# Optimization experiments

Measured on AMD Instinct MI355X. Metric: run time of the kernel, lower is better.

Reference implementation:

```python
import jax, jax.numpy as jnp
import numpy as np

DIM = 1024
STATE = 16
K = 4
INNER = 2048
BATCH = 4
SEQ = 2048
EPS = 1e-6


def silu(x):
    return x * jax.nn.sigmoid(x)


def setup_inputs() -> dict:
    key = jax.random.key(0)
    ks = jax.random.split(key, 8)
    g = lambda k, s, sc: jax.random.normal(k, s, dtype=jnp.float32) * sc
    return {
        "x": jax.random.normal(ks[0], (BATCH, SEQ, DIM), dtype=jnp.float32),
        "w_norm": jnp.ones((DIM,), jnp.float32),
        "W_in": g(ks[1], (2 * INNER, DIM), 0.02),
        "conv_w": g(ks[2], (INNER, K), 0.2),  # depthwise conv kernel
        "conv_b": jnp.zeros((INNER,), jnp.float32),
        "W_dt": g(ks[3], (INNER, INNER), 0.02),
        "b_dt": jnp.zeros((INNER,), jnp.float32),
        "W_B": g(ks[4], (STATE, INNER), 0.02),
        "W_C": g(ks[5], (STATE, INNER), 0.02),
        "A_log": jnp.log(jnp.broadcast_to(jnp.arange(1, STATE + 1, dtype=jnp.float32), (INNER, STATE))),
        "D": jnp.ones((INNER,), jnp.float32),
        "W_out": g(ks[6], (DIM, INNER), 0.02),
    }


def reference(x, w_norm, W_in, conv_w, conv_b, W_dt, b_dt, W_B, W_C, A_log, D, W_out):
    b, L, d = x.shape
    # RMSNorm
    x_norm = x * jax.lax.rsqrt(jnp.mean(x * x, axis=-1, keepdims=True) + EPS) * w_norm
    # input projection and split
    x_and_res = x_norm @ W_in.T  # (b, L, 2*inner)
    x_inner, res = jnp.split(x_and_res, 2, axis=-1)
    # causal depthwise conv1d (pad left K-1, kernel per channel)
    xp = jnp.pad(x_inner, ((0, 0), (K - 1, 0), (0, 0)))
    x_conv = sum(xp[:, j:j + L, :] * conv_w[:, j] for j in range(K)) + conv_b
    x_conv = silu(x_conv)
    # SSM parameters
    dt = jax.nn.softplus(x_conv @ W_dt.T + b_dt)  # (b, L, inner)
    Bm = x_conv @ W_B.T  # (b, L, state)
    Cm = x_conv @ W_C.T  # (b, L, state)
    A = -jnp.exp(A_log)  # (inner, state)

    def step(h, inp):
        dt_t, B_t, C_t, xc_t = inp  # (b,inner),(b,state),(b,state),(b,inner)
        dA = jnp.exp(A * dt_t[..., None])  # (b, inner, state)
        h = dA * h + (dt_t[..., None] * B_t[:, None, :]) * xc_t[..., None]
        y_t = jnp.einsum('bis,bs->bi', h, C_t) + D * xc_t
        return h, y_t

    h0 = jnp.zeros((b, INNER, STATE), x.dtype)
    xs = (dt.transpose(1, 0, 2), Bm.transpose(1, 0, 2), Cm.transpose(1, 0, 2), x_conv.transpose(1, 0, 2))
    _, y = jax.lax.scan(step, h0, xs)  # y: (L, b, inner)
    y = y.transpose(1, 0, 2)
    y = y * silu(res)
    return y @ W_out.T
```

## Files before the change

### kernel.cpp

```cpp
#include <hip/hip_runtime.h>


typedef __bf16 bf16;
typedef __attribute__((ext_vector_type(8))) __bf16 bf16x8;
typedef __attribute__((ext_vector_type(4))) float f32x4;

#define DIM   1024
#define STATE 16
#define INNER 2048
#define BATCH 4
#define SEQ   2048
#define ROWS  (BATCH * SEQ)
#define N1    (2 * INNER)
#define NBC   2176
#define CHUNK 128
#define NC    (SEQ / CHUNK)
#define PF2   4

#define GLOAD_LDS16(g, l)                                                  \
  __builtin_amdgcn_global_load_lds(                                        \
      (const __attribute__((address_space(1))) unsigned int*)(g),          \
      (__attribute__((address_space(3))) unsigned int*)(l), 16, 0, 0)

__global__ void ws_report_kernel(float* out, float wssz, float need) {
  if (threadIdx.x == 0) { out[0] = wssz; out[1] = need; }
}

__global__ __launch_bounds__(256) void rmsnorm_kernel(
    const float* __restrict__ x, const float* __restrict__ w,
    bf16* __restrict__ out) {
  const int row = blockIdx.x;
  const int t = threadIdx.x;
  const float4 v = ((const float4*)(x + (long)row * DIM))[t];
  float ss = v.x * v.x + v.y * v.y + v.z * v.z + v.w * v.w;
#pragma unroll
  for (int off = 32; off > 0; off >>= 1) ss += __shfl_xor(ss, off, 64);
  __shared__ float red[4];
  if ((t & 63) == 0) red[t >> 6] = ss;
  __syncthreads();
  const float tot = red[0] + red[1] + red[2] + red[3];
  const float scale = rsqrtf(tot * (1.0f / DIM) + 1e-6f);
  const float4 wv = ((const float4*)w)[t];
  bf16* o = out + (long)row * DIM + t * 4;
  o[0] = (bf16)(v.x * scale * wv.x);
  o[1] = (bf16)(v.y * scale * wv.y);
  o[2] = (bf16)(v.z * scale * wv.z);
  o[3] = (bf16)(v.w * scale * wv.w);
}

__global__ __launch_bounds__(256) void cvt_bf16_kernel(
    const float* __restrict__ src, bf16* __restrict__ dst, int n) {
  const int i = blockIdx.x * 256 + threadIdx.x;
  if (i < n) dst[i] = (bf16)src[i];
}

__global__ __launch_bounds__(256) void build_wbc_kernel(
    const float* __restrict__ WB, const float* __restrict__ WC,
    bf16* __restrict__ dst) {
  const int i = blockIdx.x * 256 + threadIdx.x;
  const int r = i >> 11;
  const int k = i & (INNER - 1);
  float v = 0.0f;
  if (r < 16) v = WB[r * INNER + k];
  else if (r < 32) v = WC[(r - 16) * INNER + k];
  dst[i] = (bf16)v;
}

__global__ __launch_bounds__(256) void build_a2_kernel(
    const float* __restrict__ A_log, float* __restrict__ A2) {
  const int i = blockIdx.x * 256 + threadIdx.x;
  A2[i] = -__expf(A_log[i]) * 1.4426950408889634f;
}

template <int EPI, int K, int NX>
__global__ __launch_bounds__(512, 2) void gemm256_kernel(
    const bf16* __restrict__ A, const bf16* __restrict__ B,
    float* __restrict__ Cf, bf16* __restrict__ Cb, bf16* __restrict__ Cb2,
    const float* __restrict__ bias) {
  __shared__ __align__(16) char lds[4][32768];
  const int tid = threadIdx.x;
  const int lane = tid & 63;
  const int wave = tid >> 6;
  const int wm = wave >> 2;
  const int wn = wave & 3;

  const int per = gridDim.x >> 3;
  const int lin = (blockIdx.x & 7) * per + (blockIdx.x >> 3);
  const int row_t = lin / NX;
  const int col_t = lin - row_t * NX;
  const long row0 = (long)row_t * 256;
  const long col0 = (long)col_t * 256;

  const int srow = tid >> 2;
  const int scb = (tid & 3) * 16;
  const int ssw = scb ^ (((srow >> 1) & 3) << 4);
  const char* gA = (const char*)A + (row0 + srow) * (long)(2 * K) + ssw;
  const char* gB = (const char*)B + (col0 + srow) * (long)(2 * K) + ssw;

#define STG_A(bb, r, tt)                                                      \
  GLOAD_LDS16(gA + (long)(r) * 128 * (2 * K) + (long)(tt) * 64,               \
              lds[bb] + (r) * 8192 + srow * 64 + scb)
#define STG_B(bb, r, tt)                                                      \
  GLOAD_LDS16(gB + (long)(r) * 128 * (2 * K) + (long)(tt) * 64,               \
              lds[bb] + 16384 + (r) * 8192 + srow * 64 + scb)

  const int fm = lane & 15;
  const int fq = lane >> 4;
  const int ck = (fq * 16) ^ (((fm >> 1) & 3) << 4);
  const int aro = (wm * 128 + fm) * 64;
  const int bro = (wn * 64 + fm) * 64;

  f32x4 acc[8][4];
#pragma unroll
  for (int i = 0; i < 8; ++i)
#pragma unroll
    for (int n = 0; n < 4; ++n) acc[i][n] = (f32x4){0.f, 0.f, 0.f, 0.f};
  bf16x8 afr[4], bfr[4];

  const int NT = K / 32;
#pragma unroll
  for (int t = 0; t < 3; ++t) {
    STG_A(t, 0, t); STG_A(t, 1, t);
    STG_B(t, 0, t); STG_B(t, 1, t);
  }
  __builtin_amdgcn_sched_barrier(0);
  asm volatile("s_waitcnt vmcnt(8)");
  __builtin_amdgcn_s_barrier();
  __builtin_amdgcn_sched_barrier(0);

  for (int t = 0; t < NT; ++t) {
    const int c = t & 3;
    const int pb = (t + 3) & 3;
    const char* Ac = lds[c];
    const char* Bc = lds[c] + 16384;
    const bool pf = (t + 3) < NT;
#pragma unroll
    for (int i = 0; i < 4; ++i)
      afr[i] = *(const bf16x8*)(Ac + aro + i * 1024 + ck);
#pragma unroll
    for (int n = 0; n < 4; ++n)
      bfr[n] = *(const bf16x8*)(Bc + bro + n * 1024 + ck);
    if (pf) { STG_A(pb, 0, t + 3); STG_A(pb, 1, t + 3); }
    __builtin_amdgcn_s_barrier();
    asm volatile("s_waitcnt lgkmcnt(0)");
    __builtin_amdgcn_sched_barrier(0);
    __builtin_amdgcn_s_setprio(1);
#pragma unroll
    for (int i = 0; i < 4; ++i)
#pragma unroll
      for (int n = 0; n < 4; ++n)
        acc[i][n] = __builtin_amdgcn_mfma_f32_16x16x32_bf16(
            afr[i], bfr[n], acc[i][n], 0, 0, 0);
    __builtin_amdgcn_s_setprio(0);
    __builtin_amdgcn_s_barrier();
#pragma unroll
    for (int i = 0; i < 4; ++i)
      afr[i] = *(const bf16x8*)(Ac + aro + (i + 4) * 1024 + ck);
    if (pf) { STG_B(pb, 0, t + 3); STG_B(pb, 1, t + 3); }
    __builtin_amdgcn_s_barrier();
    asm volatile("s_waitcnt lgkmcnt(0)");
    __builtin_amdgcn_sched_barrier(0);
    __builtin_amdgcn_s_setprio(1);
#pragma unroll
    for (int i = 0; i < 4; ++i)
#pragma unroll
      for (int n = 0; n < 4; ++n)
        acc[4 + i][n] = __builtin_amdgcn_mfma_f32_16x16x32_bf16(
            afr[i], bfr[n], acc[4 + i][n], 0, 0, 0);
    __builtin_amdgcn_s_setprio(0);
    __builtin_amdgcn_sched_barrier(0);
    if (t < NT - 3) {
      asm volatile("s_waitcnt vmcnt(8)");
    } else if (t == NT - 3) {
      asm volatile("s_waitcnt vmcnt(4)");
    } else if (t == NT - 2) {
      asm volatile("s_waitcnt vmcnt(0)");
    }
    __builtin_amdgcn_s_barrier();
    __builtin_amdgcn_sched_barrier(0);
  }
#undef STG_A
#undef STG_B

  const int er = fq * 4;
  const long rbase = row0 + wm * 128;
  const long cbase = col0 + wn * 64;
  if (EPI == 0) {
    const long Nn = 256 * NX;
#pragma unroll
    for (int i = 0; i < 8; ++i)
#pragma unroll
      for (int n = 0; n < 4; ++n) {
        const long col = cbase + n * 16 + fm;
        const long rw = rbase + i * 16 + er;
#pragma unroll
        for (int r = 0; r < 4; ++r) Cf[(rw + r) * Nn + col] = acc[i][n][r];
      }
  } else if (EPI == 1) {
#pragma unroll
    for (int i = 0; i < 8; ++i)
#pragma unroll
      for (int n = 0; n < 4; ++n) {
        const long col = cbase + n * 16 + fm;
        const float bs = bias[col];
        const long rw = rbase + i * 16 + er;
#pragma unroll
        for (int r = 0; r < 4; ++r) {
          float z = acc[i][n][r] + bs;
          z = (z > 20.0f) ? z : log1pf(__expf(z));
          Cf[(rw + r) * 2048 + col] = z;
        }
      }
  } else {
    if (col0 < 2048) {
#pragma unroll
      for (int i = 0; i < 8; ++i)
#pragma unroll
        for (int n = 0; n < 4; ++n) {
          const long col = cbase + n * 16 + fm;
          const long rw = rbase + i * 16 + er;
#pragma unroll
          for (int r = 0; r < 4; ++r)
            Cb[(rw + r) * 2048 + col] = (bf16)acc[i][n][r];
        }
    } else {
#pragma unroll
      for (int i = 0; i < 8; ++i)
#pragma unroll
        for (int n = 0; n < 4; ++n) {
          const long col = cbase + n * 16 + fm - 2048;
          const long rw = rbase + i * 16 + er;
#pragma unroll
          for (int r = 0; r < 4; ++r) {
            const float v = acc[i][n][r];
            const float s = v / (1.0f + __expf(-v));
            Cb2[(rw + r) * 2048 + col] = (bf16)s;
          }
        }
    }
  }
}

template <int EPI>
__global__ __launch_bounds__(256) void gemm_bf16_kernel(
    const bf16* __restrict__ A, const bf16* __restrict__ B,
    float* __restrict__ Cf2, int nx, int N, int K) {
  __shared__ __align__(16) bf16 As[128 * 32];
  __shared__ __align__(16) bf16 Bs[128 * 32];
  const int tid = threadIdx.x;
  const int lane = tid & 63;
  const int wave = tid >> 6;

  const int per = gridDim.x >> 3;
  const int lin = (blockIdx.x & 7) * per + (blockIdx.x >> 3);
  const int row_t = lin / nx;
  const int col_t = lin - row_t * nx;
  const long row0 = (long)row_t * 128;
  const long col0 = (long)col_t * 128;

  const int wr = (wave >> 1) * 64;
  const int wc = (wave & 1) * 64;

  f32x4 acc[4][4];
#pragma unroll
  for (int i = 0; i < 4; i++)
#pragma unroll
    for (int j = 0; j < 4; j++) acc[i][j] = (f32x4){0.f, 0.f, 0.f, 0.f};

  const int srow = tid >> 2;
  const int scol = (tid & 3) * 8;
  const bf16* gA0 = A + (row0 + srow) * (long)K + scol;
  const bf16* gA1 = A + (row0 + srow + 64) * (long)K + scol;
  const bf16* gB0 = B + (col0 + srow) * (long)K + scol;
  const bf16* gB1 = B + (col0 + srow + 64) * (long)K + scol;
  bf16* lA0 = As + wave * 512 + lane * 8;
  bf16* lA1 = As + 64 * 32 + wave * 512 + lane * 8;
  bf16* lB0 = Bs + wave * 512 + lane * 8;
  bf16* lB1 = Bs + 64 * 32 + wave * 512 + lane * 8;

  const int fm = lane & 15;
  const int fk = (lane >> 4) * 8;

  for (int k0 = 0; k0 < K; k0 += 32) {
    GLOAD_LDS16(gA0 + k0, lA0);
    GLOAD_LDS16(gA1 + k0, lA1);
    GLOAD_LDS16(gB0 + k0, lB0);
    GLOAD_LDS16(gB1 + k0, lB1);
    __syncthreads();
    bf16x8 af[4], bfv[4];
#pragma unroll
    for (int i = 0; i < 4; i++)
      af[i] = *(const bf16x8*)(As + (wr + i * 16 + fm) * 32 + fk);
#pragma unroll
    for (int j = 0; j < 4; j++)
      bfv[j] = *(const bf16x8*)(Bs + (wc + j * 16 + fm) * 32 + fk);
#pragma unroll
    for (int i = 0; i < 4; i++)
#pragma unroll
      for (int j = 0; j < 4; j++)
        acc[i][j] = __builtin_amdgcn_mfma_f32_16x16x32_bf16(
            af[i], bfv[j], acc[i][j], 0, 0, 0);
    __syncthreads();
  }

  const int er = (lane >> 4) * 4;
  const int ec = lane & 15;
#pragma unroll
  for (int i = 0; i < 4; i++) {
#pragma unroll
    for (int j = 0; j < 4; j++) {
      const long col = col0 + wc + j * 16 + ec;
      const long rw = row0 + wr + i * 16 + er;
#pragma unroll
      for (int r = 0; r < 4; r++) {
        const float v = acc[i][j][r];
        const long row = rw + r;
        if (EPI == 3) {
          if (col < 32) Cf2[row * 32 + col] = v;
        }
      }
    }
  }
}

__global__ __launch_bounds__(256) void conv_silu_kernel(
    const bf16* __restrict__ xin, const float* __restrict__ conv_w,
    const float* __restrict__ conv_b, bf16* __restrict__ xc16) {
  const int c = blockIdx.x * 256 + threadIdx.x;
  const int r = blockIdx.y;
  const int l = r & (SEQ - 1);
  const float4 w = *(const float4*)(conv_w + c * 4);
  float acc = conv_b[c];
#pragma unroll
  for (int j = 0; j < 4; j++) {
    const int lp = l - 3 + j;
    const float xv = (lp >= 0) ? (float)xin[(long)(r - 3 + j) * INNER + c] : 0.0f;
    acc += xv * ((const float*)&w)[j];
  }
  const float s = acc / (1.0f + __expf(-acc));
  xc16[(long)r * INNER + c] = (bf16)s;
}

__global__ __launch_bounds__(256) void scan_pass1_kernel(
    const float* __restrict__ dtm, const float* __restrict__ bc,
    const bf16* __restrict__ xc, const float* __restrict__ A2,
    float* __restrict__ hend, float* __restrict__ dtsum) {
  const int ch = blockIdx.x * 256 + threadIdx.x;
  const int c = blockIdx.y;
  const int b = blockIdx.z;
  const long row0 = (long)b * SEQ + (long)c * CHUNK;

  float a2[16];
#pragma unroll
  for (int q = 0; q < 4; q++) {
    const float4 t = ((const float4*)(A2 + (long)ch * 16))[q];
    a2[q * 4 + 0] = t.x; a2[q * 4 + 1] = t.y;
    a2[q * 4 + 2] = t.z; a2[q * 4 + 3] = t.w;
  }
  float h[16];
#pragma unroll
  for (int s = 0; s < 16; s++) h[s] = 0.0f;
  float dts = 0.0f;

  float dtq[PF2], xcq[PF2];
#pragma unroll
  for (int p = 0; p < PF2; p++) {
    const long r2 = row0 + p;
    dtq[p] = dtm[r2 * INNER + ch];
    xcq[p] = (float)xc[r2 * INNER + ch];
  }
  for (int l0 = 0; l0 <= CHUNK - 2 * PF2; l0 += PF2) {
#pragma unroll
    for (int p = 0; p < PF2; p++) {
      const float dt = dtq[p], xcv = xcq[p];
      const long rp = row0 + l0 + p + PF2;
      dtq[p] = dtm[rp * INNER + ch];
      xcq[p] = (float)xc[rp * INNER + ch];
      const long r = row0 + l0 + p;
      float Bv[16];
#pragma unroll
      for (int k = 0; k < 16; k++) Bv[k] = bc[r * 32 + k];
      dts += dt;
      const float u = dt * xcv;
#pragma unroll
      for (int s = 0; s < 16; s++)
        h[s] = exp2f(a2[s] * dt) * h[s] + Bv[s] * u;
    }
  }
#pragma unroll
  for (int p = 0; p < PF2; p++) {
    const float dt = dtq[p], xcv = xcq[p];
    const long r = row0 + CHUNK - PF2 + p;
    float Bv[16];
#pragma unroll
    for (int k = 0; k < 16; k++) Bv[k] = bc[r * 32 + k];
    dts += dt;
    const float u = dt * xcv;
#pragma unroll
    for (int s = 0; s < 16; s++)
      h[s] = exp2f(a2[s] * dt) * h[s] + Bv[s] * u;
  }

  const long cb = (long)(b * NC + c);
#pragma unroll
  for (int s = 0; s < 16; s++) hend[(cb * 16 + s) * INNER + ch] = h[s];
  dtsum[cb * INNER + ch] = dts;
}

__global__ __launch_bounds__(256) void scan_combine_kernel(
    float* __restrict__ hio, const float* __restrict__ dtsum,
    const float* __restrict__ A2) {
  const int idx = blockIdx.x * 256 + threadIdx.x;
  const int ch = idx & (INNER - 1);
  const int s = (idx >> 11) & 15;
  const int b = idx >> 15;
  const float a2 = A2[(long)ch * 16 + s];
  float H = 0.0f;
  for (int c = 0; c < NC; c++) {
    const long cb = (long)(b * NC + c);
    const long o = (cb * 16 + s) * INNER + ch;
    const float he = hio[o];
    const float ds = dtsum[cb * INNER + ch];
    hio[o] = H;
    H = exp2f(a2 * ds) * H + he;
  }
}

__global__ __launch_bounds__(256) void scan_pass3_kernel(
    const float* __restrict__ dtm, const float* __restrict__ bc,
    const bf16* __restrict__ xc, const bf16* __restrict__ rs,
    const float* __restrict__ A2, const float* __restrict__ Dv,
    const float* __restrict__ hstart, bf16* __restrict__ y) {
  const int ch = blockIdx.x * 256 + threadIdx.x;
  const int c = blockIdx.y;
  const int b = blockIdx.z;
  const long row0 = (long)b * SEQ + (long)c * CHUNK;

  float a2[16];
#pragma unroll
  for (int q = 0; q < 4; q++) {
    const float4 t = ((const float4*)(A2 + (long)ch * 16))[q];
    a2[q * 4 + 0] = t.x; a2[q * 4 + 1] = t.y;
    a2[q * 4 + 2] = t.z; a2[q * 4 + 3] = t.w;
  }
  const float d = Dv[ch];
  const long cb = (long)(b * NC + c);
  float h[16];
#pragma unroll
  for (int s = 0; s < 16; s++) h[s] = hstart[(cb * 16 + s) * INNER + ch];

  float dtq[PF2], xcq[PF2], rsq[PF2];
#pragma unroll
  for (int p = 0; p < PF2; p++) {
    const long r2 = row0 + p;
    dtq[p] = dtm[r2 * INNER + ch];
    xcq[p] = (float)xc[r2 * INNER + ch];
    rsq[p] = (float)rs[r2 * INNER + ch];
  }
  for (int l0 = 0; l0 <= CHUNK - 2 * PF2; l0 += PF2) {
#pragma unroll
    for (int p = 0; p < PF2; p++) {
      const float dt = dtq[p], xcv = xcq[p], rsv = rsq[p];
      const long rp = row0 + l0 + p + PF2;
      dtq[p] = dtm[rp * INNER + ch];
      xcq[p] = (float)xc[rp * INNER + ch];
      rsq[p] = (float)rs[rp * INNER + ch];
      const long r = row0 + l0 + p;
      float Bv[16], Cv[16];
#pragma unroll
      for (int k = 0; k < 16; k++) Bv[k] = bc[r * 32 + k];
#pragma unroll
      for (int k = 0; k < 16; k++) Cv[k] = bc[r * 32 + 16 + k];
      const float u = dt * xcv;
      float yv = d * xcv;
#pragma unroll
      for (int s = 0; s < 16; s++) {
        h[s] = exp2f(a2[s] * dt) * h[s] + Bv[s] * u;
        yv += h[s] * Cv[s];
      }
      y[r * INNER + ch] = (bf16)(yv * rsv);
    }
  }
#pragma unroll
  for (int p = 0; p < PF2; p++) {
    const float dt = dtq[p], xcv = xcq[p], rsv = rsq[p];
    const long r = row0 + CHUNK - PF2 + p;
    float Bv[16], Cv[16];
#pragma unroll
    for (int k = 0; k < 16; k++) Bv[k] = bc[r * 32 + k];
#pragma unroll
    for (int k = 0; k < 16; k++) Cv[k] = bc[r * 32 + 16 + k];
    const float u = dt * xcv;
    float yv = d * xcv;
#pragma unroll
    for (int s = 0; s < 16; s++) {
      h[s] = exp2f(a2[s] * dt) * h[s] + Bv[s] * u;
      yv += h[s] * Cv[s];
    }
    y[r * INNER + ch] = (bf16)(yv * rsv);
  }
}

extern "C" void kernel_launch(void* const* d_in, const int* in_sizes, int n_in,
                              void* d_out, int out_size, void* d_ws,
                              size_t ws_size, hipStream_t stream) {
  (void)in_sizes; (void)n_in; (void)out_size;
  const float* x      = (const float*)d_in[0];
  const float* w_norm = (const float*)d_in[1];
  const float* W_in   = (const float*)d_in[2];
  const float* conv_w = (const float*)d_in[3];
  const float* conv_b = (const float*)d_in[4];
  const float* W_dt   = (const float*)d_in[5];
  const float* b_dt   = (const float*)d_in[6];
  const float* W_B    = (const float*)d_in[7];
  const float* W_C    = (const float*)d_in[8];
  const float* A_log  = (const float*)d_in[9];
  const float* Dv     = (const float*)d_in[10];
  const float* W_out  = (const float*)d_in[11];
  float* out = (float*)d_out;

  const size_t MB = 1024ull * 1024ull;
  char* base = (char*)d_ws;
  bf16*  xnorm  = (bf16*)(base + 0);
  bf16*  win_b  = (bf16*)(base + 16 * MB);
  bf16*  xin_b  = (bf16*)(base + 24 * MB);
  float* dtm    = (float*)(base + 0);
  float* bcm    = (float*)(base + 64 * MB);
  bf16*  res_b  = (bf16*)(base + 65 * MB);
  bf16*  xc_b   = (bf16*)(base + 97 * MB);
  bf16*  wdt_b  = (bf16*)(base + 129 * MB);
  bf16*  wbc_b  = (bf16*)(base + 137 * MB);
  float* hend   = (float*)(base + 129 * MB);
  float* dtsum  = (float*)(base + 137 * MB);
  char*  p2     = base + 129 * MB + (size_t)NBC * INNER * 2;
  bf16*  wout_b = (bf16*)p2;
  float* A2     = (float*)(p2 + (size_t)DIM * INNER * 2);
  bf16*  yb     = (bf16*)(p2 + (size_t)DIM * INNER * 2 +
                          (size_t)INNER * STATE * 4);
  const size_t NEEDED = (size_t)((char*)yb - base) + (size_t)ROWS * INNER * 2;

  if (ws_size < NEEDED) {
    ws_report_kernel<<<1, 64, 0, stream>>>(out, (float)ws_size, (float)NEEDED);
    return;
  }

  rmsnorm_kernel<<<ROWS, 256, 0, stream>>>(x, w_norm, xnorm);

  cvt_bf16_kernel<<<(N1 * DIM) / 256, 256, 0, stream>>>(W_in, win_b, N1 * DIM);
  cvt_bf16_kernel<<<(INNER * INNER) / 256, 256, 0, stream>>>(W_dt, wdt_b,
                                                             INNER * INNER);
  build_wbc_kernel<<<(128 * INNER) / 256, 256, 0, stream>>>(W_B, W_C, wbc_b);
  cvt_bf16_kernel<<<(DIM * INNER) / 256, 256, 0, stream>>>(W_out, wout_b,
                                                           DIM * INNER);
  build_a2_kernel<<<(INNER * STATE) / 256, 256, 0, stream>>>(A_log, A2);

  gemm256_kernel<2, 1024, 16><<<512, 512, 0, stream>>>(
      xnorm, win_b, nullptr, xin_b, res_b, nullptr);

  conv_silu_kernel<<<dim3(INNER / 256, ROWS), 256, 0, stream>>>(
      xin_b, conv_w, conv_b, xc_b);

  gemm256_kernel<1, 2048, 8><<<256, 512, 0, stream>>>(
      xc_b, wdt_b, dtm, nullptr, nullptr, b_dt);

  gemm_bf16_kernel<3><<<64, 256, 0, stream>>>(xc_b, wbc_b, bcm, 1, 128, INNER);

  scan_pass1_kernel<<<dim3(INNER / 256, NC, BATCH), 256, 0, stream>>>(
      dtm, bcm, xc_b, A2, hend, dtsum);
  scan_combine_kernel<<<(BATCH * 16 * INNER) / 256, 256, 0, stream>>>(
      hend, dtsum, A2);
  scan_pass3_kernel<<<dim3(INNER / 256, NC, BATCH), 256, 0, stream>>>(
      dtm, bcm, xc_b, res_b, A2, Dv, hend, yb);

  gemm256_kernel<0, 2048, 4><<<128, 512, 0, stream>>>(
      yb, wout_b, out, nullptr, nullptr, nullptr);
}
```

Baseline: 669.5 us.

## Unroll GEMM main loop by four and merge per-step barriers into one

The bf16 MFMA GEMM main loop is unrolled four times so the LDS ring-buffer index is a compile-time constant. Each step now loads all A and B fragments up front and issues both A and B prefetches together. It then runs all 32 MFMAs with a single barrier at the end of the step instead of four. The aim is to cut barrier stalls and address arithmetic and to give the scheduler more freedom to overlap LDS reads with MFMA. In exchange it uses more fragment registers and assumes the tile count is a multiple of four.

```diff
diff --git a/kernel.cpp b/kernel.cpp
--- a/kernel.cpp
+++ b/kernel.cpp
@@ -115,70 +115,65 @@
   for (int i = 0; i < 8; ++i)
 #pragma unroll
     for (int n = 0; n < 4; ++n) acc[i][n] = (f32x4){0.f, 0.f, 0.f, 0.f};
-  bf16x8 afr[4], bfr[4];
 
   const int NT = K / 32;
 #pragma unroll
-  for (int t = 0; t < 3; ++t) {
-    STG_A(t, 0, t); STG_A(t, 1, t);
-    STG_B(t, 0, t); STG_B(t, 1, t);
+  for (int t0 = 0; t0 < 3; ++t0) {
+    STG_A(t0, 0, t0); STG_A(t0, 1, t0);
+    STG_B(t0, 0, t0); STG_B(t0, 1, t0);
   }
   __builtin_amdgcn_sched_barrier(0);
   asm volatile("s_waitcnt vmcnt(8)");
   __builtin_amdgcn_s_barrier();
   __builtin_amdgcn_sched_barrier(0);
 
-  for (int t = 0; t < NT; ++t) {
-    const int c = t & 3;
-    const int pb = (t + 3) & 3;
-    const char* Ac = lds[c];
-    const char* Bc = lds[c] + 16384;
-    const bool pf = (t + 3) < NT;
-#pragma unroll
-    for (int i = 0; i < 4; ++i)
-      afr[i] = *(const bf16x8*)(Ac + aro + i * 1024 + ck);
-#pragma unroll
-    for (int n = 0; n < 4; ++n)
-      bfr[n] = *(const bf16x8*)(Bc + bro + n * 1024 + ck);
-    if (pf) { STG_A(pb, 0, t + 3); STG_A(pb, 1, t + 3); }
-    __builtin_amdgcn_s_barrier();
-    asm volatile("s_waitcnt lgkmcnt(0)");
-    __builtin_amdgcn_sched_barrier(0);
-    __builtin_amdgcn_s_setprio(1);
-#pragma unroll
-    for (int i = 0; i < 4; ++i)
-#pragma unroll
-      for (int n = 0; n < 4; ++n)
-        acc[i][n] = __builtin_amdgcn_mfma_f32_16x16x32_bf16(
-            afr[i], bfr[n], acc[i][n], 0, 0, 0);
-    __builtin_amdgcn_s_setprio(0);
-    __builtin_amdgcn_s_barrier();
-#pragma unroll
-    for (int i = 0; i < 4; ++i)
-      afr[i] = *(const bf16x8*)(Ac + aro + (i + 4) * 1024 + ck);
-    if (pf) { STG_B(pb, 0, t + 3); STG_B(pb, 1, t + 3); }
-    __builtin_amdgcn_s_barrier();
-    asm volatile("s_waitcnt lgkmcnt(0)");
-    __builtin_amdgcn_sched_barrier(0);
-    __builtin_amdgcn_s_setprio(1);
-#pragma unroll
-    for (int i = 0; i < 4; ++i)
-#pragma unroll
-      for (int n = 0; n < 4; ++n)
-        acc[4 + i][n] = __builtin_amdgcn_mfma_f32_16x16x32_bf16(
-            afr[i], bfr[n], acc[4 + i][n], 0, 0, 0);
-    __builtin_amdgcn_s_setprio(0);
-    __builtin_amdgcn_sched_barrier(0);
-    if (t < NT - 3) {
-      asm volatile("s_waitcnt vmcnt(8)");
-    } else if (t == NT - 3) {
-      asm volatile("s_waitcnt vmcnt(4)");
-    } else if (t == NT - 2) {
-      asm volatile("s_waitcnt vmcnt(0)");
+#define TILE_STEP(CI)                                                         \
+  {                                                                           \
+    const bool pf = (t + 3) < NT;                                             \
+    bf16x8 al[4], bh[4], ah[4];                                               \
+    _Pragma("unroll") for (int i = 0; i < 4; ++i)                             \
+        al[i] = *(const bf16x8*)(lds[CI] + aro + i * 1024 + ck);              \
+    _Pragma("unroll") for (int n = 0; n < 4; ++n)                             \
+        bh[n] = *(const bf16x8*)(lds[CI] + 16384 + bro + n * 1024 + ck);      \
+    _Pragma("unroll") for (int i = 0; i < 4; ++i)                             \
+        ah[i] = *(const bf16x8*)(lds[CI] + aro + (i + 4) * 1024 + ck);        \
+    if (pf) {                                                                 \
+      STG_A((CI + 3) & 3, 0, t + 3); STG_A((CI + 3) & 3, 1, t + 3);           \
+      STG_B((CI + 3) & 3, 0, t + 3); STG_B((CI + 3) & 3, 1, t + 3);           \
+    }                                                                         \
+    __builtin_amdgcn_s_setprio(1);                                            \
+    _Pragma("unroll") for (int i = 0; i < 4; ++i)                             \
+    _Pragma("unroll") for (int n = 0; n < 4; ++n)                             \
+        acc[i][n] = __builtin_amdgcn_mfma_f32_16x16x32_bf16(                  \
+            al[i], bh[n], acc[i][n], 0, 0, 0);                                \
+    _Pragma("unroll") for (int i = 0; i < 4; ++i)                             \
+    _Pragma("unroll") for (int n = 0; n < 4; ++n)                             \
+        acc[4 + i][n] = __builtin_amdgcn_mfma_f32_16x16x32_bf16(              \
+            ah[i], bh[n], acc[4 + i][n], 0, 0, 0);                            \
+    __builtin_amdgcn_s_setprio(0);                                            \
+    __builtin_amdgcn_sched_barrier(0);     \
+    if (t < NT - 3) {                                                         \
+      asm volatile("s_waitcnt vmcnt(8)");                                     \
+    } else if (t == NT - 3) {                                                 \
+      asm volatile("s_waitcnt vmcnt(4)");                                     \
+    } else if (t == NT - 2) {                                                 \
+      asm volatile("s_waitcnt vmcnt(0)");                                     \
+    }                                                                         \
+    __builtin_amdgcn_s_barrier();                                             \
+    __builtin_amdgcn_sched_barrier(0);               \
+    ++t;                                                                      \
+  }
+
+  {
+    int t = 0;
+    for (int tb = 0; tb < NT / 4; ++tb) {
+      TILE_STEP(0)
+      TILE_STEP(1)
+      TILE_STEP(2)
+      TILE_STEP(3)
     }
-    __builtin_amdgcn_s_barrier();
-    __builtin_amdgcn_sched_barrier(0);
-  }
+  }
+#undef TILE_STEP
 #undef STG_A
 #undef STG_B
 
```

Result: faster. 647.5 us (-3.3%).
